# Kernel optimization log

Measured on AMD Instinct MI355X. Metric: run time of the kernel, lower is better.

Reference implementation:

```python
import jax, jax.numpy as jnp
import numpy as np

N_NODES = 100000
N_EDGES = 1600000
D = 64


def _ngcf_conv(x, W1, W2, src, dst, n_nodes):
    """One NGCF graph conv layer.

    out_i = W1 x_i + sum_{(j->i) in E} 1/sqrt(d_j d_i) * (W1 x_j + W2 (x_j * x_i))
    Degrees are computed from the edge list (min-clipped to 1).
    """
    ones = jnp.ones(src.shape[0], dtype=x.dtype)
    deg_out = jnp.clip(jax.ops.segment_sum(ones, src, num_segments=n_nodes), 1.0)
    deg_in = jnp.clip(jax.ops.segment_sum(ones, dst, num_segments=n_nodes), 1.0)
    norm = jax.lax.rsqrt(deg_out[src] * deg_in[dst])  # [E]

    h_src = x[src]                      # [E, D] gather
    h_dst = x[dst]                      # [E, D] gather
    msg = (h_src @ W1 + (h_src * h_dst) @ W2) * norm[:, None]  # [E, D]
    agg = jax.ops.segment_sum(msg, dst, num_segments=n_nodes)  # [N, D] scatter-add
    return x @ W1 + agg


def setup_inputs() -> dict:
    key = jax.random.key(0)
    ks = jax.random.split(key, 8)
    s = 1.0 / np.sqrt(D)
    return {
        "x": jax.random.normal(ks[0], (N_NODES, D), dtype=jnp.float32),
        "edge_src": jax.random.randint(ks[1], (N_EDGES,), 0, N_NODES, dtype=jnp.int32),
        "edge_dst": jax.random.randint(ks[2], (N_EDGES,), 0, N_NODES, dtype=jnp.int32),
        "W1_1": jax.random.normal(ks[3], (D, D), dtype=jnp.float32) * s,
        "W2_1": jax.random.normal(ks[4], (D, D), dtype=jnp.float32) * s,
        "W1_2": jax.random.normal(ks[5], (D, D), dtype=jnp.float32) * s,
        "W2_2": jax.random.normal(ks[6], (D, D), dtype=jnp.float32) * s,
    }


def reference(x, edge_src, edge_dst, W1_1, W2_1, W1_2, W2_2):
    n = x.shape[0]
    h = _ngcf_conv(x, W1_1, W2_1, edge_src, edge_dst, n)
    h = jax.nn.relu(h)
    h = _ngcf_conv(h, W1_2, W2_2, edge_src, edge_dst, n)
    return h
```

## Files before the change

### kernel.cpp

```cpp
#include <hip/hip_runtime.h>

#define D 64
#define SCAN_CHUNK 1024
#define MAX_CHUNKS 128
#define BSHIFT 9
#define BNODES (1 << BSHIFT)
#define CHUNK 8192

__device__ int g_partials[MAX_CHUNKS];

__global__ __launch_bounds__(256) void scanA(const int* __restrict__ cnt, int n) {
    __shared__ int red[256];
    int b = blockIdx.x, t = threadIdx.x;
    int base = b * SCAN_CHUNK + t * 4;
    int s = 0;
#pragma unroll
    for (int j = 0; j < 4; ++j) {
        int i = base + j;
        if (i < n) s += cnt[i];
    }
    red[t] = s;
    __syncthreads();
    for (int off = 128; off > 0; off >>= 1) {
        if (t < off) red[t] += red[t + off];
        __syncthreads();
    }
    if (t == 0) g_partials[b] = red[0];
}

__global__ __launch_bounds__(128) void scanB(int nchunks) {
    __shared__ int sh[MAX_CHUNKS];
    int t = threadIdx.x;
    int v = (t < nchunks) ? g_partials[t] : 0;
    sh[t] = v;
    __syncthreads();
    for (int off = 1; off < MAX_CHUNKS; off <<= 1) {
        int a = (t >= off) ? sh[t - off] : 0;
        __syncthreads();
        sh[t] += a;
        __syncthreads();
    }
    if (t < nchunks) g_partials[t] = sh[t] - v;
}

__global__ __launch_bounds__(256) void scanC(const int* __restrict__ cnt,
                                             int* __restrict__ offs, int n) {
    __shared__ int sums[256];
    int b = blockIdx.x, t = threadIdx.x;
    int base = b * SCAN_CHUNK + t * 4;
    int v[4];
    int tot = 0;
#pragma unroll
    for (int j = 0; j < 4; ++j) {
        int i = base + j;
        v[j] = (i < n) ? cnt[i] : 0;
        tot += v[j];
    }
    sums[t] = tot;
    __syncthreads();
    for (int off = 1; off < 256; off <<= 1) {
        int a = (t >= off) ? sums[t - off] : 0;
        __syncthreads();
        sums[t] += a;
        __syncthreads();
    }
    int run = sums[t] - tot + g_partials[b];
#pragma unroll
    for (int j = 0; j < 4; ++j) {
        int i = base + j;
        if (i < n) offs[i] = run;
        run += v[j];
    }
}

__global__ __launch_bounds__(256) void partAB(const int* __restrict__ src,
                                              const int* __restrict__ dst,
                                              int* __restrict__ histJ,
                                              int E, int G, int NB, int HL) {
    __shared__ int hD[256], hS[256];
    int g = blockIdx.x;
    hD[threadIdx.x] = 0;
    hS[threadIdx.x] = 0;
    __syncthreads();
    int base = g * CHUNK;
    int lim = min(E - base, CHUNK);
    for (int i = threadIdx.x; i < lim; i += 256) {
        atomicAdd(&hD[dst[base + i] >> BSHIFT], 1);
        atomicAdd(&hS[src[base + i] >> BSHIFT], 1);
    }
    __syncthreads();
    if (threadIdx.x < NB) {
        histJ[threadIdx.x * G + g] = hD[threadIdx.x];
        histJ[HL + threadIdx.x * G + g] = hS[threadIdx.x];
    }
}

__global__ __launch_bounds__(256) void partCJ(const int* __restrict__ src,
                                              const int* __restrict__ dst,
                                              const int* __restrict__ histJs,
                                              int* __restrict__ ebufS, int* __restrict__ ebufD,
                                              int* __restrict__ ebufK,
                                              int E, int G, int NB, int HL) {
    __shared__ int curD[256], curK[256];
    int g = blockIdx.x;
    if (threadIdx.x < NB) {
        curD[threadIdx.x] = histJs[threadIdx.x * G + g];
        curK[threadIdx.x] = histJs[HL + threadIdx.x * G + g];
    }
    __syncthreads();
    int base = g * CHUNK;
    int lim = min(E - base, CHUNK);
    for (int i = threadIdx.x; i < lim; i += 256) {
        int d = dst[base + i];
        int s = src[base + i];
        int pD = atomicAdd(&curD[d >> BSHIFT], 1);
        ebufS[pD] = s;
        ebufD[pD] = d;
        int pK = atomicAdd(&curK[s >> BSHIFT], 1) - E;
        ebufK[pK] = s;
    }
}

__global__ __launch_bounds__(256) void partDcount(const int* __restrict__ ebufD,
                                                  const int* __restrict__ ebufK,
                                                  const int* __restrict__ histJs,
                                                  int* __restrict__ cnt_dst, float* __restrict__ rs_src,
                                                  int E, int G, int NB, int HL, int N) {
    __shared__ int cntD[BNODES], cntS[BNODES];
    int b = blockIdx.x;
    int nbase = b << BSHIFT;
    for (int i = threadIdx.x; i < BNODES; i += 256) { cntD[i] = 0; cntS[i] = 0; }
    __syncthreads();
    int dS = histJs[b * G];
    int dE = (b + 1 < NB) ? histJs[(b + 1) * G] : E;
    for (int p = dS + threadIdx.x; p < dE; p += 256)
        atomicAdd(&cntD[ebufD[p] - nbase], 1);
    int kS = histJs[HL + b * G] - E;
    int kE = (b + 1 < NB) ? histJs[HL + (b + 1) * G] - E : E;
    for (int p = kS + threadIdx.x; p < kE; p += 256)
        atomicAdd(&cntS[ebufK[p] - nbase], 1);
    __syncthreads();
    for (int i = threadIdx.x; i < BNODES; i += 256) {
        int node = nbase + i;
        if (node < N) {
            cnt_dst[node] = cntD[i];
            rs_src[node] = rsqrtf((float)max(cntS[i], 1));
        }
    }
}

__global__ __launch_bounds__(256) void partD2(const int* __restrict__ ebufS,
                                              const int* __restrict__ ebufD,
                                              const int* __restrict__ histJs,
                                              const int* __restrict__ offs,
                                              int* __restrict__ sortedSrc,
                                              int E, int G, int NB, int N) {
    __shared__ int cur[BNODES];
    int b = blockIdx.x;
    int nbase = b << BSHIFT;
    for (int i = threadIdx.x; i < BNODES; i += 256) {
        int node = nbase + i;
        cur[i] = (node < N) ? offs[node] : 0;
    }
    __syncthreads();
    int dS = histJs[b * G];
    int dE = (b + 1 < NB) ? histJs[(b + 1) * G] : E;
    for (int p = dS + threadIdx.x; p < dE; p += 256) {
        int d = ebufD[p];
        int s = ebufS[p];
        int pos = atomicAdd(&cur[d - nbase], 1);
        sortedSrc[pos] = s;
    }
}

__global__ __launch_bounds__(256) void gather_kernel(
    const int* __restrict__ offs, const int* __restrict__ cnt_dst,
    const int* __restrict__ sortedSrc, const float* __restrict__ rs_src,
    const float* __restrict__ X, float* __restrict__ S, int n) {
    int lane = threadIdx.x & 63;
    int node = blockIdx.x * 4 + (threadIdx.x >> 6);
    if (node >= n) return;
    int start = offs[node];
    int cnt = cnt_dst[node];
    int end = start + cnt;
    float acc = 0.0f;
    int p = start;
    for (; p + 8 <= end; p += 8) {
        int idx[8];
        float w[8];
        float r[8];
#pragma unroll
        for (int j = 0; j < 8; ++j) idx[j] = sortedSrc[p + j];
#pragma unroll
        for (int j = 0; j < 8; ++j) w[j] = rs_src[idx[j]];
#pragma unroll
        for (int j = 0; j < 8; ++j) r[j] = X[(size_t)idx[j] * D + lane];
#pragma unroll
        for (int j = 0; j < 8; ++j) acc = fmaf(w[j], r[j], acc);
    }
    if (p < end) {
        int idx[8];
        float w[8];
        float r[8];
#pragma unroll
        for (int j = 0; j < 8; ++j) {
            int q = p + j;
            int qc = (q < end) ? q : (end - 1);
            idx[j] = sortedSrc[qc];
        }
#pragma unroll
        for (int j = 0; j < 8; ++j) w[j] = (p + j < end) ? rs_src[idx[j]] : 0.0f;
#pragma unroll
        for (int j = 0; j < 8; ++j) r[j] = X[(size_t)idx[j] * D + lane];
#pragma unroll
        for (int j = 0; j < 8; ++j) acc = fmaf(w[j], r[j], acc);
    }
    float rd = rsqrtf((float)max(cnt, 1));
    S[(size_t)node * D + lane] = acc * rd;
}

__global__ __launch_bounds__(256, 4) void combine_kernel(
    const float* X, const float* S,
    const float* __restrict__ W1, const float* __restrict__ W2,
    float* Out, int n, int relu_flag) {
    __shared__ float xs[64][65];
    __shared__ float ss[64][65];
    int t = threadIdx.x;
    int rowBase = blockIdx.x * 64;
    int lane = t & 63;
    int wv = __builtin_amdgcn_readfirstlane(t >> 6);
    int q = t & 15;
    int sr = t >> 4;

#pragma unroll
    for (int p = 0; p < 4; ++p) {
        int r = p * 16 + sr;
        int g = min(rowBase + r, n - 1);
        float4 xv = *(const float4*)(X + (size_t)g * D + q * 4);
        float4 sv = *(const float4*)(S + (size_t)g * D + q * 4);
        int c = q * 4;
        xs[r][c + 0] = xv.x; xs[r][c + 1] = xv.y;
        xs[r][c + 2] = xv.z; xs[r][c + 3] = xv.w;
        ss[r][c + 0] = sv.x; ss[r][c + 1] = sv.y;
        ss[r][c + 2] = sv.z; ss[r][c + 3] = sv.w;
    }
    __syncthreads();

    float4 A0 = make_float4(0.f, 0.f, 0.f, 0.f);
    float4 A1 = A0, A2 = A0, A3 = A0;
    const float* W1c = W1 + wv * 16;
    const float* W2c = W2 + wv * 16;
#pragma unroll 2
    for (int j = 0; j < 64; ++j) {
        float xk = xs[lane][j];
        float sk = ss[lane][j];
        float u = xk + sk;
        float v = xk * sk;
        float4 w10 = *(const float4*)(W1c + j * D + 0);
        float4 w11 = *(const float4*)(W1c + j * D + 4);
        float4 w12 = *(const float4*)(W1c + j * D + 8);
        float4 w13 = *(const float4*)(W1c + j * D + 12);
        float4 w20 = *(const float4*)(W2c + j * D + 0);
        float4 w21 = *(const float4*)(W2c + j * D + 4);
        float4 w22 = *(const float4*)(W2c + j * D + 8);
        float4 w23 = *(const float4*)(W2c + j * D + 12);
        A0.x = fmaf(u, w10.x, fmaf(v, w20.x, A0.x));
        A0.y = fmaf(u, w10.y, fmaf(v, w20.y, A0.y));
        A0.z = fmaf(u, w10.z, fmaf(v, w20.z, A0.z));
        A0.w = fmaf(u, w10.w, fmaf(v, w20.w, A0.w));
        A1.x = fmaf(u, w11.x, fmaf(v, w21.x, A1.x));
        A1.y = fmaf(u, w11.y, fmaf(v, w21.y, A1.y));
        A1.z = fmaf(u, w11.z, fmaf(v, w21.z, A1.z));
        A1.w = fmaf(u, w11.w, fmaf(v, w21.w, A1.w));
        A2.x = fmaf(u, w12.x, fmaf(v, w22.x, A2.x));
        A2.y = fmaf(u, w12.y, fmaf(v, w22.y, A2.y));
        A2.z = fmaf(u, w12.z, fmaf(v, w22.z, A2.z));
        A2.w = fmaf(u, w12.w, fmaf(v, w22.w, A2.w));
        A3.x = fmaf(u, w13.x, fmaf(v, w23.x, A3.x));
        A3.y = fmaf(u, w13.y, fmaf(v, w23.y, A3.y));
        A3.z = fmaf(u, w13.z, fmaf(v, w23.z, A3.z));
        A3.w = fmaf(u, w13.w, fmaf(v, w23.w, A3.w));
    }

    int row0 = rowBase + lane;
    if (row0 < n) {
        if (relu_flag) {
            A0.x = fmaxf(A0.x, 0.f); A0.y = fmaxf(A0.y, 0.f);
            A0.z = fmaxf(A0.z, 0.f); A0.w = fmaxf(A0.w, 0.f);
            A1.x = fmaxf(A1.x, 0.f); A1.y = fmaxf(A1.y, 0.f);
            A1.z = fmaxf(A1.z, 0.f); A1.w = fmaxf(A1.w, 0.f);
            A2.x = fmaxf(A2.x, 0.f); A2.y = fmaxf(A2.y, 0.f);
            A2.z = fmaxf(A2.z, 0.f); A2.w = fmaxf(A2.w, 0.f);
            A3.x = fmaxf(A3.x, 0.f); A3.y = fmaxf(A3.y, 0.f);
            A3.z = fmaxf(A3.z, 0.f); A3.w = fmaxf(A3.w, 0.f);
        }
        float4* o4 = (float4*)(Out + (size_t)row0 * D + wv * 16);
        o4[0] = A0; o4[1] = A1; o4[2] = A2; o4[3] = A3;
    }
}

extern "C" void kernel_launch(void* const* d_in, const int* in_sizes, int n_in,
                              void* d_out, int out_size, void* d_ws, size_t ws_size,
                              hipStream_t stream) {
    const float* x    = (const float*)d_in[0];
    const int*   src  = (const int*)d_in[1];
    const int*   dst  = (const int*)d_in[2];
    const float* W1_1 = (const float*)d_in[3];
    const float* W2_1 = (const float*)d_in[4];
    const float* W1_2 = (const float*)d_in[5];
    const float* W2_2 = (const float*)d_in[6];
    float* out = (float*)d_out;

    const int N = in_sizes[0] / D;
    const int E = in_sizes[1];

    const int NB = (N + BNODES - 1) >> BSHIFT;
    const int G  = (E + CHUNK - 1) / CHUNK;
    const int HL = NB * G;

    int*   cnt_dst   = (int*)d_ws;
    int*   offs      = cnt_dst + N;
    float* rs_src    = (float*)(cnt_dst + 2 * (size_t)N);
    int*   sortedSrc = cnt_dst + 3 * (size_t)N;
    int*   histJ     = sortedSrc + E;
    int*   histJs    = histJ + 2 * (size_t)HL;
    float* S         = (float*)(histJs + 2 * (size_t)HL);
    int*   ebufS     = (int*)S;
    int*   ebufD     = ebufS + E;
    int*   ebufK     = ebufD + E;

    const int tb = 256;
    const int g_blocks = (N + 3) / 4;
    const int c_blocks = (N + 63) / 64;
    const int nchunksN = (N + SCAN_CHUNK - 1) / SCAN_CHUNK;
    const int nchunksJ = (2 * HL + SCAN_CHUNK - 1) / SCAN_CHUNK;

    partAB<<<G, tb, 0, stream>>>(src, dst, histJ, E, G, NB, HL);
    scanA<<<nchunksJ, tb, 0, stream>>>(histJ, 2 * HL);
    scanB<<<1, 128, 0, stream>>>(nchunksJ);
    scanC<<<nchunksJ, tb, 0, stream>>>(histJ, histJs, 2 * HL);

    partCJ<<<G, tb, 0, stream>>>(src, dst, histJs, ebufS, ebufD, ebufK, E, G, NB, HL);

    partDcount<<<NB, tb, 0, stream>>>(ebufD, ebufK, histJs, cnt_dst, rs_src, E, G, NB, HL, N);

    scanA<<<nchunksN, tb, 0, stream>>>(cnt_dst, N);
    scanB<<<1, 128, 0, stream>>>(nchunksN);
    scanC<<<nchunksN, tb, 0, stream>>>(cnt_dst, offs, N);

    partD2<<<NB, tb, 0, stream>>>(ebufS, ebufD, histJs, offs, sortedSrc, E, G, NB, N);

    gather_kernel<<<g_blocks, tb, 0, stream>>>(offs, cnt_dst, sortedSrc, rs_src, x, S, N);
    combine_kernel<<<c_blocks, tb, 0, stream>>>(x, S, W1_1, W2_1, out, N, 1);

    gather_kernel<<<g_blocks, tb, 0, stream>>>(offs, cnt_dst, sortedSrc, rs_src, out, S, N);
    combine_kernel<<<c_blocks, tb, 0, stream>>>(out, S, W1_2, W2_2, out, N, 0);
}
```

Baseline: 368.1 us.

## Pack edge weights with sorted sources and gather two nodes per wave

The CSR build now stores each edge's source index together with its precomputed source rsqrt-degree weight as an int2. The gather no longer does a dependent random load of rs_src per edge. The gather kernel also splits each 64-lane wave into two halves, one node per half, and each lane loads a float2, so each wave runs two neighbour lists in parallel. The cost is double the size of the sorted edge array, and divergence when the two paired nodes have different degrees.

```diff
diff --git a/kernel.cpp b/kernel.cpp
--- a/kernel.cpp
+++ b/kernel.cpp
@@ -153,7 +153,8 @@
                                               const int* __restrict__ ebufD,
                                               const int* __restrict__ histJs,
                                               const int* __restrict__ offs,
-                                              int* __restrict__ sortedSrc,
+                                              const float* __restrict__ rs_src,
+                                              int2* __restrict__ sortedEW,
                                               int E, int G, int NB, int N) {
     __shared__ int cur[BNODES];
     int b = blockIdx.x;
@@ -168,55 +169,68 @@
     for (int p = dS + threadIdx.x; p < dE; p += 256) {
         int d = ebufD[p];
         int s = ebufS[p];
+        float w = rs_src[s];
         int pos = atomicAdd(&cur[d - nbase], 1);
-        sortedSrc[pos] = s;
+        sortedEW[pos] = make_int2(s, __float_as_int(w));
     }
 }
 
 __global__ __launch_bounds__(256) void gather_kernel(
     const int* __restrict__ offs, const int* __restrict__ cnt_dst,
-    const int* __restrict__ sortedSrc, const float* __restrict__ rs_src,
+    const int2* __restrict__ sortedEW,
     const float* __restrict__ X, float* __restrict__ S, int n) {
-    int lane = threadIdx.x & 63;
-    int node = blockIdx.x * 4 + (threadIdx.x >> 6);
-    if (node >= n) return;
-    int start = offs[node];
-    int cnt = cnt_dst[node];
+    int t = threadIdx.x;
+    int lane = t & 63;
+    int half = lane >> 5;
+    int col2 = (lane & 31) * 2;
+    int wid = blockIdx.x * (blockDim.x >> 6) + (t >> 6);
+    int node = wid * 2 + half;
+    int nc = min(node, n - 1);
+    int start = offs[nc];
+    int cnt = (node < n) ? cnt_dst[nc] : 0;
     int end = start + cnt;
-    float acc = 0.0f;
-    int p = start;
-    for (; p + 8 <= end; p += 8) {
-        int idx[8];
-        float w[8];
-        float r[8];
-#pragma unroll
-        for (int j = 0; j < 8; ++j) idx[j] = sortedSrc[p + j];
-#pragma unroll
-        for (int j = 0; j < 8; ++j) w[j] = rs_src[idx[j]];
-#pragma unroll
-        for (int j = 0; j < 8; ++j) r[j] = X[(size_t)idx[j] * D + lane];
-#pragma unroll
-        for (int j = 0; j < 8; ++j) acc = fmaf(w[j], r[j], acc);
-    }
-    if (p < end) {
-        int idx[8];
-        float w[8];
-        float r[8];
-#pragma unroll
-        for (int j = 0; j < 8; ++j) {
-            int q = p + j;
-            int qc = (q < end) ? q : (end - 1);
-            idx[j] = sortedSrc[qc];
-        }
-#pragma unroll
-        for (int j = 0; j < 8; ++j) w[j] = (p + j < end) ? rs_src[idx[j]] : 0.0f;
-#pragma unroll
-        for (int j = 0; j < 8; ++j) r[j] = X[(size_t)idx[j] * D + lane];
-#pragma unroll
-        for (int j = 0; j < 8; ++j) acc = fmaf(w[j], r[j], acc);
-    }
-    float rd = rsqrtf((float)max(cnt, 1));
-    S[(size_t)node * D + lane] = acc * rd;
+    int cntO = __shfl_xor(cnt, 32, 64);
+    int cmin = min(cnt, cntO);
+    int cmax = max(cnt, cntO);
+
+    float2 acc = make_float2(0.f, 0.f);
+    const float* Xc = X + col2;
+    int j = 0;
+    for (; j + 8 <= cmin; j += 8) {
+        int2 ew[8];
+#pragma unroll
+        for (int u = 0; u < 8; ++u) ew[u] = sortedEW[start + j + u];
+        float2 r[8];
+#pragma unroll
+        for (int u = 0; u < 8; ++u) r[u] = *(const float2*)(Xc + (size_t)ew[u].x * D);
+#pragma unroll
+        for (int u = 0; u < 8; ++u) {
+            float w = __int_as_float(ew[u].y);
+            acc.x = fmaf(w, r[u].x, acc.x);
+            acc.y = fmaf(w, r[u].y, acc.y);
+        }
+    }
+    for (; j < cmax; j += 8) {
+        int2 ew[8];
+#pragma unroll
+        for (int u = 0; u < 8; ++u) {
+            int qc = max(min(start + j + u, end - 1), 0);
+            ew[u] = sortedEW[qc];
+        }
+        float2 r[8];
+#pragma unroll
+        for (int u = 0; u < 8; ++u) r[u] = *(const float2*)(Xc + (size_t)ew[u].x * D);
+#pragma unroll
+        for (int u = 0; u < 8; ++u) {
+            float w = (j + u < cnt) ? __int_as_float(ew[u].y) : 0.0f;
+            acc.x = fmaf(w, r[u].x, acc.x);
+            acc.y = fmaf(w, r[u].y, acc.y);
+        }
+    }
+    if (node < n) {
+        float rd = rsqrtf((float)max(cnt, 1));
+        *(float2*)(S + (size_t)node * D + col2) = make_float2(acc.x * rd, acc.y * rd);
+    }
 }
 
 __global__ __launch_bounds__(256, 4) void combine_kernel(
@@ -321,8 +335,8 @@
     int*   cnt_dst   = (int*)d_ws;
     int*   offs      = cnt_dst + N;
     float* rs_src    = (float*)(cnt_dst + 2 * (size_t)N);
-    int*   sortedSrc = cnt_dst + 3 * (size_t)N;
-    int*   histJ     = sortedSrc + E;
+    int2*  sortedEW  = (int2*)(cnt_dst + 3 * (size_t)N);
+    int*   histJ     = (int*)(sortedEW + E);
     int*   histJs    = histJ + 2 * (size_t)HL;
     float* S         = (float*)(histJs + 2 * (size_t)HL);
     int*   ebufS     = (int*)S;
@@ -330,7 +344,7 @@
     int*   ebufK     = ebufD + E;
 
     const int tb = 256;
-    const int g_blocks = (N + 3) / 4;
+    const int g_blocks = (N / 2 + 3) / 4 + 1;
     const int c_blocks = (N + 63) / 64;
     const int nchunksN = (N + SCAN_CHUNK - 1) / SCAN_CHUNK;
     const int nchunksJ = (2 * HL + SCAN_CHUNK - 1) / SCAN_CHUNK;
@@ -348,11 +362,11 @@
     scanB<<<1, 128, 0, stream>>>(nchunksN);
     scanC<<<nchunksN, tb, 0, stream>>>(cnt_dst, offs, N);
 
-    partD2<<<NB, tb, 0, stream>>>(ebufS, ebufD, histJs, offs, sortedSrc, E, G, NB, N);
-
-    gather_kernel<<<g_blocks, tb, 0, stream>>>(offs, cnt_dst, sortedSrc, rs_src, x, S, N);
+    partD2<<<NB, tb, 0, stream>>>(ebufS, ebufD, histJs, offs, rs_src, sortedEW, E, G, NB, N);
+
+    gather_kernel<<<g_blocks, tb, 0, stream>>>(offs, cnt_dst, sortedEW, x, S, N);
     combine_kernel<<<c_blocks, tb, 0, stream>>>(x, S, W1_1, W2_1, out, N, 1);
 
-    gather_kernel<<<g_blocks, tb, 0, stream>>>(offs, cnt_dst, sortedSrc, rs_src, out, S, N);
+    gather_kernel<<<g_blocks, tb, 0, stream>>>(offs, cnt_dst, sortedEW, out, S, N);
     combine_kernel<<<c_blocks, tb, 0, stream>>>(out, S, W1_2, W2_2, out, N, 0);
 }
```

Measured after the change: 381.3 us. 1.04x slower.
